# Optimization experiments

Measured on AMD Instinct MI355X. Metric: run time of the kernel, lower is better.

The kernel has to match this reference:

```python
import jax, jax.numpy as jnp
import numpy as np
from jax import lax

NUM_MASK_PARAMS = 67  # 66 weights (64 feat + 2 coord channels) + 1 bias
NUM_GEN_PARAMS = 134


def _coord_maps(h, w, dtype):
    yy = jnp.broadcast_to(jnp.linspace(-1.0, 1.0, h, dtype=dtype)[:, None], (h, w))
    xx = jnp.broadcast_to(jnp.linspace(-1.0, 1.0, w, dtype=dtype)[None, :], (h, w))
    return xx, yy


def _dynamic_head(x_cat, p):
    # x_cat: [66, H, W]; p: [num_ins, 67] -> [num_ins, H, W]
    w = p[:, :NUM_MASK_PARAMS - 1]
    b = p[:, NUM_MASK_PARAMS - 1]
    return jnp.einsum('ic,chw->ihw', w, x_cat) + b[:, None, None]


def setup_inputs() -> dict:
    key = jax.random.key(0)
    ks = jax.random.split(key, 10)
    C, HM, WM, HH, WH, MB, HID = 256, 272, 480, 136, 240, 64, 64
    rn = lambda k, s, sc=1.0: jax.random.normal(k, s, dtype=jnp.float32) * sc
    return {
        'out0': rn(ks[0], (1, C, HM, WM)),
        'out1': rn(ks[1], (1, C, HH, WH)),
        'hm_w': rn(ks[2], (1, C), 0.05),
        'hm_b': jnp.zeros((1,), jnp.float32),
        'params_w': rn(ks[3], (NUM_GEN_PARAMS, C), 0.05),
        'params_b': rn(ks[4], (NUM_GEN_PARAMS,), 0.05),
        'mb_w': rn(ks[5], (MB, C, 3, 3), 0.05),
        'mb_b': jnp.zeros((MB,), jnp.float32),
        'mlp_w1': rn(ks[6], (HM, HID), 0.05),
        'mlp_b1': jnp.zeros((HID,), jnp.float32),
        'mlp_w2': rn(ks[7], (HID, 2), 0.05),
        'mlp_b2': jnp.zeros((2,), jnp.float32),
        'num_ins': 4,
    }


def reference(out0, out1, hm_w, hm_b, params_w, params_b, mb_w, mb_b,
              mlp_w1, mlp_b1, mlp_w2, mlp_b2, num_ins):
    h_mask, w_mask = out0.shape[2], out0.shape[3]
    h_hm, w_hm = out1.shape[2], out1.shape[3]

    # ctnet head: 1x1 convs on the stride-16 feature
    hm = jnp.einsum('kc,bchw->bkhw', hm_w, out1) + hm_b[None, :, None, None]
    params = jnp.einsum('kc,bchw->bkhw', params_w, out1) + params_b[None, :, None, None]
    hm = jnp.clip(jax.nn.sigmoid(hm), 1e-4, 1.0 - 1e-4)  # [1,1,h_hm,w_hm]
    # [1,134,h,w] -> [h*w, 134]
    params_flat = jnp.transpose(params[0], (1, 2, 0)).reshape(-1, NUM_GEN_PARAMS)

    # 3x3 maxpool NMS (stride 1, pad 1), keep only local peaks
    hmax = lax.reduce_window(hm, -jnp.inf, lax.max, (1, 1, 3, 3), (1, 1, 1, 1),
                             [(0, 0), (0, 0), (1, 1), (1, 1)])
    keep = (hmax == hm).astype(hm.dtype)
    heat_nms = (hm * keep).reshape(-1)

    scores, inds = lax.top_k(heat_nms, num_ins)

    # mask branch: 3x3 conv + relu on the stride-8 feature
    mask_branch = lax.conv_general_dilated(out0, mb_w, (1, 1), 'SAME',
                                           dimension_numbers=('NCHW', 'OIHW', 'NCHW'))
    mask_branch = jax.nn.relu(mask_branch + mb_b[None, :, None, None])  # [1,64,H,W]

    xx, yy = _coord_maps(h_mask, w_mask, mask_branch.dtype)
    x_cat = jnp.concatenate([mask_branch[0], xx[None], yy[None]], axis=0)  # [66,H,W]

    gen_params = params_flat[inds]  # [num_ins, 134]
    masks0 = _dynamic_head(x_cat, gen_params[:, :NUM_MASK_PARAMS])   # [num_ins,H,W]
    regs0 = _dynamic_head(x_cat, gen_params[:, NUM_MASK_PARAMS:])    # [num_ins,H,W]

    # row-wise vertical-range MLP over h_mask
    feat_range = jnp.transpose(masks0, (0, 2, 1))  # [num_ins, w_mask, h_mask]
    h1 = jax.nn.relu(feat_range @ mlp_w1 + mlp_b1)
    feat_range = h1 @ mlp_w2 + mlp_b2  # [num_ins, w_mask, 2]

    return scores, inds, regs0, masks0, feat_range
```

## Files before the change

### kernel.cpp

```cpp
#include <hip/hip_runtime.h>
#include <math.h>
#include <limits.h>

#define C_IN 256
#define HM_H 136
#define HM_W 240
#define HM_N (HM_H * HM_W)
#define MB   64
#define MH   272
#define MW   480
#define MN   (MH * MW)
#define NP   134
#define NI   4
#define HID  64

#define REG_OFF   8
#define MASK_OFF  (8 + NI * MN)
#define FEAT_OFF  (8 + 2 * NI * MN)

#define WS_HM   0
#define WS_CV   HM_N
#define WS_CI   (HM_N + 512)
#define WS_GP   (2 * HM_N)
#define WS_WT_F 65824

typedef float  f32x4  __attribute__((ext_vector_type(4)));
typedef short  bf16x8 __attribute__((ext_vector_type(8)));
typedef unsigned short u16x4 __attribute__((ext_vector_type(4)));

__device__ __forceinline__ unsigned short f2bf(float f) {
  unsigned int u = __float_as_uint(f);
  u += 0x7FFFu + ((u >> 16) & 1u);
  return (unsigned short)(u >> 16);
}
__device__ __forceinline__ float b2f(unsigned short h) {
  return __uint_as_float(((unsigned int)h) << 16);
}

__global__ void k_prep(const float* __restrict__ mb_w, unsigned short* __restrict__ wt,
                       const float* __restrict__ out1, const float* __restrict__ hm_w,
                       const float* __restrict__ hm_b, float* __restrict__ ws_hm) {
  __shared__ float part[4][64];
  if (blockIdx.x < 576) {
    int idx = blockIdx.x * 256 + threadIdx.x;
    int j    = idx & 7;
    int lane = (idx >> 3) & 63;
    int nt   = (idx >> 9) & 3;
    int gt   = idx >> 11;
    int t    = gt % 9;
    int g    = gt / 9;
    int n = nt * 16 + (lane & 15);
    int c = g * 32 + (lane >> 4) * 8 + j;
    wt[idx] = f2bf(mb_w[(n * C_IN + c) * 9 + t]);
  } else {
    int b = blockIdx.x - 576, t = threadIdx.x;
    int cg = t >> 6, pl = t & 63;
    int p = b * 64 + pl;
    float s = 0.f;
    #pragma unroll 16
    for (int c = 0; c < 64; ++c)
      s += hm_w[cg * 64 + c] * out1[(cg * 64 + c) * HM_N + p];
    part[cg][pl] = s;
    __syncthreads();
    if (t < 64) {
      float tot = part[0][t] + part[1][t] + part[2][t] + part[3][t] + hm_b[0];
      float sig = 1.f / (1.f + expf(-tot));
      sig = fminf(fmaxf(sig, 1e-4f), 1.f - 1e-4f);
      ws_hm[b * 64 + t] = sig;
    }
  }
}

__device__ __forceinline__ bool better(float av, int ai, float bv, int bi) {
  return (av > bv) || (av == bv && ai < bi);
}

template<int NTHR>
__device__ void top4_tree(float* sv, int* si, int t) {
  for (int s = NTHR / 2; s >= 1; s >>= 1) {
    if (t < s) {
      float a[4], b[4]; int ai[4], bj[4];
      #pragma unroll
      for (int k = 0; k < 4; ++k) {
        a[k] = sv[t * 4 + k];        ai[k] = si[t * 4 + k];
        b[k] = sv[(t + s) * 4 + k];  bj[k] = si[(t + s) * 4 + k];
      }
      float ov[4]; int oi[4];
      int i = 0, j = 0;
      #pragma unroll
      for (int k = 0; k < 4; ++k) {
        if (better(a[i], ai[i], b[j], bj[j])) { ov[k] = a[i]; oi[k] = ai[i]; ++i; }
        else                                   { ov[k] = b[j]; oi[k] = bj[j]; ++j; }
      }
      #pragma unroll
      for (int k = 0; k < 4; ++k) { sv[t * 4 + k] = ov[k]; si[t * 4 + k] = oi[k]; }
    }
    __syncthreads();
  }
}

__global__ void k_nms_top(const float* __restrict__ ws_hm, float* __restrict__ candv,
                          int* __restrict__ candi) {
  __shared__ float sv[256 * 4];
  __shared__ int   si[256 * 4];
  int b = blockIdx.x, t = threadIdx.x;
  float v = -1.f; int idx = INT_MAX;
  if (t < 255) {
    int p = b * 255 + t;
    int y = p / HM_W, x = p - y * HM_W;
    float c = ws_hm[p], m = c;
    #pragma unroll
    for (int dy = -1; dy <= 1; ++dy)
      #pragma unroll
      for (int dx = -1; dx <= 1; ++dx) {
        int yy = y + dy, xx = x + dx;
        if (yy >= 0 && yy < HM_H && xx >= 0 && xx < HM_W)
          m = fmaxf(m, ws_hm[yy * HM_W + xx]);
      }
    v = (c == m) ? c : 0.f;
    idx = p;
  }
  sv[t * 4] = v; si[t * 4] = idx;
  #pragma unroll
  for (int k = 1; k < 4; ++k) { sv[t * 4 + k] = -1.f; si[t * 4 + k] = INT_MAX; }
  __syncthreads();
  top4_tree<256>(sv, si, t);
  if (t == 0) {
    #pragma unroll
    for (int k = 0; k < 4; ++k) { candv[b * 4 + k] = sv[k]; candi[b * 4 + k] = si[k]; }
  }
}

__global__ void k_gen(const float* __restrict__ candv, const int* __restrict__ candi,
                      const float* __restrict__ out1, const float* __restrict__ params_w,
                      const float* __restrict__ params_b, float* __restrict__ ws_gp,
                      float* __restrict__ d_out) {
  __shared__ float sv[128 * 4];
  __shared__ int   si[128 * 4];
  __shared__ float col[C_IN];
  int t = threadIdx.x, i = blockIdx.x;
  if (t < 128) {
    #pragma unroll
    for (int k = 0; k < 4; ++k) { sv[t * 4 + k] = candv[t * 4 + k]; si[t * 4 + k] = candi[t * 4 + k]; }
  }
  __syncthreads();
  top4_tree<128>(sv, si, t);
  if (i == 0 && t < 4) {
    d_out[t]     = sv[t];
    d_out[4 + t] = (float)si[t];
  }
  int p = si[i];
  col[t] = out1[t * HM_N + p];
  __syncthreads();
  if (t < NP) {
    float s = params_b[t];
    #pragma unroll 8
    for (int c = 0; c < C_IN; ++c) s += params_w[t * C_IN + c] * col[c];
    ws_gp[i * NP + t] = s;
  }
}

#define CSU 32
#define RP  36
#define BUFU (10 * RP * CSU)

__device__ __forceinline__ void stage_store(unsigned short* buf, const f32x4* dq,
                                            bool gv, const int* lw, unsigned sm) {
  #pragma unroll
  for (int e = 0; e < 4; ++e) if ((sm >> e) & 1u) {
    u16x4 v;
    v[0] = f2bf(gv ? dq[0][e] : 0.f);
    v[1] = f2bf(gv ? dq[1][e] : 0.f);
    v[2] = f2bf(gv ? dq[2][e] : 0.f);
    v[3] = f2bf(gv ? dq[3][e] : 0.f);
    *(u16x4*)(buf + lw[e]) = v;
  }
}

__global__ __launch_bounds__(512, 3) void k_conv_mfma(
    const float* __restrict__ out0, const unsigned short* __restrict__ wt,
    const float* __restrict__ mb_b, const float* __restrict__ ws_gp,
    float* __restrict__ d_out) {
  __shared__ unsigned short smem[2 * BUFU];

  int tid  = threadIdx.x;
  int lane = tid & 63;
  int wv   = tid >> 6;
  int n15  = lane & 15;
  int kq   = lane >> 4;
  int gx0 = blockIdx.x * 32, gy0 = blockIdx.y * 8;

  int goff[2]; int lws[2][4]; unsigned smask[2]; bool gvld[2];
  #pragma unroll
  for (int kk = 0; kk < 2; ++kk) {
    int u = tid + 512 * kk;
    bool uv = (u < 800);
    int uu = uv ? u : 0;
    int cq  = uu / 100;
    int rem = uu - cq * 100;
    int row = rem / 10;
    int qx  = rem - row * 10;
    int iy  = gy0 + row - 1;
    int ixq = gx0 + 4 * qx - 4;
    bool v = uv && (iy >= 0) && (iy < MH) && (ixq >= 0) && (ixq + 3 < MW);
    gvld[kk] = v;
    goff[kk] = v ? (cq * 4 * MN + iy * MW + ixq) : 0;
    unsigned sm = 0;
    #pragma unroll
    for (int e = 0; e < 4; ++e) {
      int sx = 4 * qx - 3 + e;
      bool s = uv && (sx >= 0) && (sx < RP);
      int sxc = s ? sx : 0;
      int pix = row * RP + sxc;
      int w2  = (pix ^ (pix >> 2)) & 3;
      lws[kk][e] = s ? ((pix << 5) + ((cq ^ (w2 << 1)) << 2)) : 0;
      if (s) sm |= (1u << e);
    }
    smask[kk] = sm;
  }

  int lrd[9];
  #pragma unroll
  for (int t = 0; t < 9; ++t) {
    int ty = t / 3, tx = t - ty * 3;
    int pix = (wv + ty) * RP + n15 + tx;
    int w2  = (pix ^ (pix >> 2)) & 3;
    lrd[t] = (pix << 5) + ((kq ^ w2) << 3);
  }

  {
    f32x4 dq[4];
    {
      const float* sp = out0 + goff[0];
      #pragma unroll
      for (int j = 0; j < 4; ++j) dq[j] = *(const f32x4*)(sp + j * MN);
      stage_store(smem, dq, gvld[0], lws[0], smask[0]);
    }
    if (tid < 288) {
      const float* sp = out0 + goff[1];
      #pragma unroll
      for (int j = 0; j < 4; ++j) dq[j] = *(const f32x4*)(sp + j * MN);
      stage_store(smem, dq, gvld[1], lws[1], smask[1]);
    }
  }
  __syncthreads();

  f32x4 acc[2][4];
  #pragma unroll
  for (int i = 0; i < 2; ++i)
    #pragma unroll
    for (int nt = 0; nt < 4; ++nt)
      acc[i][nt] = (f32x4){0.f, 0.f, 0.f, 0.f};

  #pragma unroll 1
  for (int g = 0; g < 8; ++g) {
    const unsigned short* cur = smem + (g & 1) * BUFU;
    unsigned short*       nxt = smem + ((g + 1) & 1) * BUFU;
    const float*          src = out0 + (g + 1) * (32 * MN);
    f32x4 dqa[4], dqb[4];

    if (g < 7) {
      const float* sp = src + goff[0];
      #pragma unroll
      for (int j = 0; j < 4; ++j) dqa[j] = *(const f32x4*)(sp + j * MN);
    }
    #pragma unroll
    for (int t = 0; t < 4; ++t) {
      const unsigned short* wb = wt + (g * 9 + t) * 2048 + lane * 8;
      bf16x8 bf[4];
      #pragma unroll
      for (int nt = 0; nt < 4; ++nt) bf[nt] = *(const bf16x8*)(wb + nt * 512);
      bf16x8 a0 = *(const bf16x8*)&cur[lrd[t]];
      bf16x8 a1 = *(const bf16x8*)&cur[lrd[t] + 512];
      #pragma unroll
      for (int nt = 0; nt < 4; ++nt) {
        acc[0][nt] = __builtin_amdgcn_mfma_f32_16x16x32_bf16(a0, bf[nt], acc[0][nt], 0, 0, 0);
        acc[1][nt] = __builtin_amdgcn_mfma_f32_16x16x32_bf16(a1, bf[nt], acc[1][nt], 0, 0, 0);
      }
    }
    if (g < 7) {
      stage_store(nxt, dqa, gvld[0], lws[0], smask[0]);
      if (tid < 288) {
        const float* sp = src + goff[1];
        #pragma unroll
        for (int j = 0; j < 4; ++j) dqb[j] = *(const f32x4*)(sp + j * MN);
      }
    }
    #pragma unroll
    for (int t = 4; t < 9; ++t) {
      const unsigned short* wb = wt + (g * 9 + t) * 2048 + lane * 8;
      bf16x8 bf[4];
      #pragma unroll
      for (int nt = 0; nt < 4; ++nt) bf[nt] = *(const bf16x8*)(wb + nt * 512);
      bf16x8 a0 = *(const bf16x8*)&cur[lrd[t]];
      bf16x8 a1 = *(const bf16x8*)&cur[lrd[t] + 512];
      #pragma unroll
      for (int nt = 0; nt < 4; ++nt) {
        acc[0][nt] = __builtin_amdgcn_mfma_f32_16x16x32_bf16(a0, bf[nt], acc[0][nt], 0, 0, 0);
        acc[1][nt] = __builtin_amdgcn_mfma_f32_16x16x32_bf16(a1, bf[nt], acc[1][nt], 0, 0, 0);
      }
    }
    if (g < 7 && tid < 288) stage_store(nxt, dqb, gvld[1], lws[1], smask[1]);
    __syncthreads();
  }

  #define ES 66
  {
    float bias[4];
    #pragma unroll
    for (int nt = 0; nt < 4; ++nt) bias[nt] = mb_b[nt * 16 + n15];
    #pragma unroll
    for (int i = 0; i < 2; ++i) {
      int pbase = wv * 32 + i * 16;
      #pragma unroll
      for (int nt = 0; nt < 4; ++nt)
        #pragma unroll
        for (int reg = 0; reg < 4; ++reg) {
          float vv = fmaxf(acc[i][nt][reg] + bias[nt], 0.f);
          smem[(pbase + kq * 4 + reg) * ES + nt * 16 + n15] = f2bf(vv);
        }
    }
  }
  __syncthreads();

  int p = tid & 255, hh = tid >> 8;
  int ob = hh * 32;
  float mres[4] = {0.f, 0.f, 0.f, 0.f};
  float rres[4] = {0.f, 0.f, 0.f, 0.f};
  #pragma unroll 8
  for (int o = 0; o < 32; ++o) {
    float v = b2f(smem[p * ES + ob + o]);
    #pragma unroll
    for (int i = 0; i < 4; ++i) {
      mres[i] += ws_gp[i * NP + ob + o] * v;
      rres[i] += ws_gp[i * NP + 67 + ob + o] * v;
    }
  }
  float* pf = (float*)smem + 8704;
  if (hh) {
    #pragma unroll
    for (int i = 0; i < 4; ++i) { pf[p * 8 + i] = mres[i]; pf[p * 8 + 4 + i] = rres[i]; }
  }
  __syncthreads();
  if (!hh) {
    int r = p >> 5, xcol = p & 31;
    int gy = gy0 + r, gx = gx0 + xcol;
    float xc = -1.f + (2.f / 479.f) * (float)gx;
    float yc = -1.f + (2.f / 271.f) * (float)gy;
    int pix = gy * MW + gx;
    #pragma unroll
    for (int i = 0; i < 4; ++i) {
      const float* gp = ws_gp + i * NP;
      d_out[MASK_OFF + i * MN + pix] = mres[i] + pf[p * 8 + i]     + gp[66]  + gp[64]  * xc + gp[65]  * yc;
      d_out[REG_OFF  + i * MN + pix] = rres[i] + pf[p * 8 + 4 + i] + gp[133] + gp[131] * xc + gp[132] * yc;
    }
  }
}

__global__ void k_mlp(const float* __restrict__ masks0, const float* __restrict__ w1,
                      const float* __restrict__ b1, const float* __restrict__ w2,
                      const float* __restrict__ b2, float* __restrict__ d_out) {
  int blk = blockIdx.x;
  int i = blk / MW;
  int w = blk - i * MW;
  int k = threadIdx.x;
  const float* mcol = masks0 + i * MN + w;
  float s = b1[k];
  #pragma unroll 4
  for (int h = 0; h < MH; ++h) s += mcol[h * MW] * w1[h * HID + k];
  s = fmaxf(s, 0.f);
  float o0 = s * w2[k * 2 + 0];
  float o1 = s * w2[k * 2 + 1];
  #pragma unroll
  for (int off = 32; off >= 1; off >>= 1) {
    o0 += __shfl_down(o0, off);
    o1 += __shfl_down(o1, off);
  }
  if (k == 0) {
    d_out[FEAT_OFF + blk * 2 + 0] = o0 + b2[0];
    d_out[FEAT_OFF + blk * 2 + 1] = o1 + b2[1];
  }
}

extern "C" void kernel_launch(void* const* d_in, const int* in_sizes, int n_in,
                              void* d_out, int out_size, void* d_ws, size_t ws_size,
                              hipStream_t stream) {
  const float* out0     = (const float*)d_in[0];
  const float* out1     = (const float*)d_in[1];
  const float* hm_w     = (const float*)d_in[2];
  const float* hm_b     = (const float*)d_in[3];
  const float* params_w = (const float*)d_in[4];
  const float* params_b = (const float*)d_in[5];
  const float* mb_w     = (const float*)d_in[6];
  const float* mb_b     = (const float*)d_in[7];
  const float* mlp_w1   = (const float*)d_in[8];
  const float* mlp_b1   = (const float*)d_in[9];
  const float* mlp_w2   = (const float*)d_in[10];
  const float* mlp_b2   = (const float*)d_in[11];

  float* ws      = (float*)d_ws;
  float* ws_hm   = ws + WS_HM;
  float* candv   = ws + WS_CV;
  int*   candi   = (int*)(ws + WS_CI);
  float* ws_gp   = ws + WS_GP;
  unsigned short* ws_wt = (unsigned short*)(ws + WS_WT_F);
  float* out     = (float*)d_out;

  k_prep<<<1086, 256, 0, stream>>>(mb_w, ws_wt, out1, hm_w, hm_b, ws_hm);
  k_nms_top<<<128, 256, 0, stream>>>(ws_hm, candv, candi);
  k_gen<<<NI, 256, 0, stream>>>(candv, candi, out1, params_w, params_b, ws_gp, out);
  dim3 gconv(MW / 32, MH / 8);
  k_conv_mfma<<<gconv, 512, 0, stream>>>(out0, ws_wt, mb_b, ws_gp, out);
  k_mlp<<<NI * MW, 64, 0, stream>>>(out + MASK_OFF, mlp_w1, mlp_b1, mlp_w2, mlp_b2, out);
}
```

Measured before the change: 343.5 us.

## Retile conv MFMA waves across channels and batch 8 columns per MLP block

```diff
diff --git a/kernel.cpp b/kernel.cpp
--- a/kernel.cpp
+++ b/kernel.cpp
@@ -26,7 +26,7 @@
 
 typedef float  f32x4  __attribute__((ext_vector_type(4)));
 typedef short  bf16x8 __attribute__((ext_vector_type(8)));
-typedef unsigned short u16x4 __attribute__((ext_vector_type(4)));
+typedef unsigned short u16x8 __attribute__((ext_vector_type(8)));
 
 __device__ __forceinline__ unsigned short f2bf(float f) {
   unsigned int u = __float_as_uint(f);
@@ -160,24 +160,41 @@
   }
 }
 
-#define CSU 32
-#define RP  36
-#define BUFU (10 * RP * CSU)
-
-__device__ __forceinline__ void stage_store(unsigned short* buf, const f32x4* dq,
-                                            bool gv, const int* lw, unsigned sm) {
+#define RP   36
+#define BUFU (10 * RP * 32)
+
+__device__ __forceinline__ void stage_store8(unsigned short* buf, const f32x4* dq,
+                                             bool gv, const int* lw, unsigned sm) {
   #pragma unroll
   for (int e = 0; e < 4; ++e) if ((sm >> e) & 1u) {
-    u16x4 v;
-    v[0] = f2bf(gv ? dq[0][e] : 0.f);
-    v[1] = f2bf(gv ? dq[1][e] : 0.f);
-    v[2] = f2bf(gv ? dq[2][e] : 0.f);
-    v[3] = f2bf(gv ? dq[3][e] : 0.f);
-    *(u16x4*)(buf + lw[e]) = v;
-  }
-}
-
-__global__ __launch_bounds__(512, 3) void k_conv_mfma(
+    u16x8 v;
+    #pragma unroll
+    for (int j = 0; j < 8; ++j) v[j] = f2bf(gv ? dq[j][e] : 0.f);
+    *(u16x8*)(buf + lw[e]) = v;
+  }
+}
+
+#define MFMA_TAPS(B, T0)                                                         \
+  _Pragma("unroll")                                                              \
+  for (int tt = 0; tt < 3; ++tt) {                                               \
+    unsigned pk = lrdp[(T0) + tt];                                               \
+    const unsigned short* c0 = cur + (pk & 0xFFFFu);                             \
+    const unsigned short* c1 = cur + (pk >> 16);                                 \
+    bf16x8 a0 = *(const bf16x8*)c0;                                              \
+    bf16x8 a1 = *(const bf16x8*)(c0 + 512);                                      \
+    bf16x8 a2 = *(const bf16x8*)c1;                                              \
+    bf16x8 a3 = *(const bf16x8*)(c1 + 512);                                      \
+    acc[0][0] = __builtin_amdgcn_mfma_f32_16x16x32_bf16(a0, B[tt][0], acc[0][0], 0, 0, 0); \
+    acc[0][1] = __builtin_amdgcn_mfma_f32_16x16x32_bf16(a0, B[tt][1], acc[0][1], 0, 0, 0); \
+    acc[1][0] = __builtin_amdgcn_mfma_f32_16x16x32_bf16(a1, B[tt][0], acc[1][0], 0, 0, 0); \
+    acc[1][1] = __builtin_amdgcn_mfma_f32_16x16x32_bf16(a1, B[tt][1], acc[1][1], 0, 0, 0); \
+    acc[2][0] = __builtin_amdgcn_mfma_f32_16x16x32_bf16(a2, B[tt][0], acc[2][0], 0, 0, 0); \
+    acc[2][1] = __builtin_amdgcn_mfma_f32_16x16x32_bf16(a2, B[tt][1], acc[2][1], 0, 0, 0); \
+    acc[3][0] = __builtin_amdgcn_mfma_f32_16x16x32_bf16(a3, B[tt][0], acc[3][0], 0, 0, 0); \
+    acc[3][1] = __builtin_amdgcn_mfma_f32_16x16x32_bf16(a3, B[tt][1], acc[3][1], 0, 0, 0); \
+  }
+
+__global__ __launch_bounds__(512, 4) void k_conv_mfma(
     const float* __restrict__ out0, const unsigned short* __restrict__ wt,
     const float* __restrict__ mb_b, const float* __restrict__ ws_gp,
     float* __restrict__ d_out) {
@@ -188,68 +205,63 @@
   int wv   = tid >> 6;
   int n15  = lane & 15;
   int kq   = lane >> 4;
+  int pg   = wv & 3;
+  int ce   = wv >> 2;
   int gx0 = blockIdx.x * 32, gy0 = blockIdx.y * 8;
 
-  int goff[2]; int lws[2][4]; unsigned smask[2]; bool gvld[2];
-  #pragma unroll
-  for (int kk = 0; kk < 2; ++kk) {
-    int u = tid + 512 * kk;
-    bool uv = (u < 800);
-    int uu = uv ? u : 0;
-    int cq  = uu / 100;
-    int rem = uu - cq * 100;
-    int row = rem / 10;
-    int qx  = rem - row * 10;
-    int iy  = gy0 + row - 1;
-    int ixq = gx0 + 4 * qx - 4;
-    bool v = uv && (iy >= 0) && (iy < MH) && (ixq >= 0) && (ixq + 3 < MW);
-    gvld[kk] = v;
-    goff[kk] = v ? (cq * 4 * MN + iy * MW + ixq) : 0;
-    unsigned sm = 0;
-    #pragma unroll
-    for (int e = 0; e < 4; ++e) {
-      int sx = 4 * qx - 3 + e;
-      bool s = uv && (sx >= 0) && (sx < RP);
-      int sxc = s ? sx : 0;
-      int pix = row * RP + sxc;
-      int w2  = (pix ^ (pix >> 2)) & 3;
-      lws[kk][e] = s ? ((pix << 5) + ((cq ^ (w2 << 1)) << 2)) : 0;
-      if (s) sm |= (1u << e);
-    }
-    smask[kk] = sm;
-  }
-
-  int lrd[9];
+  bool act = tid < 400;
+  int u    = act ? tid : 0;
+  int co8  = u / 100;
+  int rem  = u - co8 * 100;
+  int row  = rem / 10;
+  int qx   = rem - row * 10;
+  int iy   = gy0 + row - 1;
+  int ixq  = gx0 + 4 * qx - 4;
+  bool gvld = act && (iy >= 0) && (iy < MH) && (ixq >= 0) && (ixq + 3 < MW);
+  int goff  = gvld ? (co8 * 8 * MN + iy * MW + ixq) : 0;
+  int lws[4]; unsigned smask = 0;
+  #pragma unroll
+  for (int e = 0; e < 4; ++e) {
+    int sx = 4 * qx - 3 + e;
+    bool sv = act && (sx >= 0) && (sx < RP);
+    int pixw = row * RP + (sv ? sx : 0);
+    int w2 = (pixw ^ (pixw >> 2)) & 3;
+    int q  = (pixw ^ row) & 1;
+    lws[e] = (pixw >> 1) * 64 + ((co8 ^ w2) << 4) + q * 8;
+    if (sv) smask |= (1u << e);
+  }
+
+  unsigned lrdp[9];
   #pragma unroll
   for (int t = 0; t < 9; ++t) {
     int ty = t / 3, tx = t - ty * 3;
-    int pix = (wv + ty) * RP + n15 + tx;
-    int w2  = (pix ^ (pix >> 2)) & 3;
-    lrd[t] = (pix << 5) + ((kq ^ w2) << 3);
+    int sr0 = pg * 2 + ty;
+    int pix0 = sr0 * RP + n15 + tx;
+    int w20 = (pix0 ^ (pix0 >> 2)) & 3;
+    int q0  = (pix0 ^ sr0) & 1;
+    unsigned o0 = (pix0 >> 1) * 64 + ((kq ^ w20) << 4) + q0 * 8;
+    int sr1 = sr0 + 1;
+    int pix1 = sr1 * RP + n15 + tx;
+    int w21 = (pix1 ^ (pix1 >> 2)) & 3;
+    int q1  = (pix1 ^ sr1) & 1;
+    unsigned o1 = (pix1 >> 1) * 64 + ((kq ^ w21) << 4) + q1 * 8;
+    lrdp[t] = o0 | (o1 << 16);
   }
 
   {
-    f32x4 dq[4];
-    {
-      const float* sp = out0 + goff[0];
-      #pragma unroll
-      for (int j = 0; j < 4; ++j) dq[j] = *(const f32x4*)(sp + j * MN);
-      stage_store(smem, dq, gvld[0], lws[0], smask[0]);
-    }
-    if (tid < 288) {
-      const float* sp = out0 + goff[1];
-      #pragma unroll
-      for (int j = 0; j < 4; ++j) dq[j] = *(const f32x4*)(sp + j * MN);
-      stage_store(smem, dq, gvld[1], lws[1], smask[1]);
-    }
-  }
-  __syncthreads();
-
-  f32x4 acc[2][4];
-  #pragma unroll
-  for (int i = 0; i < 2; ++i)
-    #pragma unroll
-    for (int nt = 0; nt < 4; ++nt)
+    f32x4 dq[8];
+    const float* sp = out0 + goff;
+    #pragma unroll
+    for (int j = 0; j < 8; ++j) dq[j] = *(const f32x4*)(sp + j * MN);
+    stage_store8(smem, dq, gvld, lws, smask);
+  }
+  __syncthreads();
+
+  f32x4 acc[4][2];
+  #pragma unroll
+  for (int i = 0; i < 4; ++i)
+    #pragma unroll
+    for (int nt = 0; nt < 2; ++nt)
       acc[i][nt] = (f32x4){0.f, 0.f, 0.f, 0.f};
 
   #pragma unroll 1
@@ -257,67 +269,59 @@
     const unsigned short* cur = smem + (g & 1) * BUFU;
     unsigned short*       nxt = smem + ((g + 1) & 1) * BUFU;
     const float*          src = out0 + (g + 1) * (32 * MN);
-    f32x4 dqa[4], dqb[4];
-
+    const unsigned short* wg_ = wt + g * (9 * 2048) + ce * 1024 + lane * 8;
+
+    bf16x8 b0[3][2], b1[3][2];
+    #pragma unroll
+    for (int tt = 0; tt < 3; ++tt) {
+      b0[tt][0] = *(const bf16x8*)(wg_ + tt * 2048);
+      b0[tt][1] = *(const bf16x8*)(wg_ + tt * 2048 + 512);
+    }
+    #pragma unroll
+    for (int tt = 0; tt < 3; ++tt) {
+      b1[tt][0] = *(const bf16x8*)(wg_ + (3 + tt) * 2048);
+      b1[tt][1] = *(const bf16x8*)(wg_ + (3 + tt) * 2048 + 512);
+    }
+    __builtin_amdgcn_sched_barrier(0);
+    f32x4 dq[8];
     if (g < 7) {
-      const float* sp = src + goff[0];
-      #pragma unroll
-      for (int j = 0; j < 4; ++j) dqa[j] = *(const f32x4*)(sp + j * MN);
-    }
-    #pragma unroll
-    for (int t = 0; t < 4; ++t) {
-      const unsigned short* wb = wt + (g * 9 + t) * 2048 + lane * 8;
-      bf16x8 bf[4];
-      #pragma unroll
-      for (int nt = 0; nt < 4; ++nt) bf[nt] = *(const bf16x8*)(wb + nt * 512);
-      bf16x8 a0 = *(const bf16x8*)&cur[lrd[t]];
-      bf16x8 a1 = *(const bf16x8*)&cur[lrd[t] + 512];
-      #pragma unroll
-      for (int nt = 0; nt < 4; ++nt) {
-        acc[0][nt] = __builtin_amdgcn_mfma_f32_16x16x32_bf16(a0, bf[nt], acc[0][nt], 0, 0, 0);
-        acc[1][nt] = __builtin_amdgcn_mfma_f32_16x16x32_bf16(a1, bf[nt], acc[1][nt], 0, 0, 0);
-      }
-    }
-    if (g < 7) {
-      stage_store(nxt, dqa, gvld[0], lws[0], smask[0]);
-      if (tid < 288) {
-        const float* sp = src + goff[1];
-        #pragma unroll
-        for (int j = 0; j < 4; ++j) dqb[j] = *(const f32x4*)(sp + j * MN);
-      }
-    }
-    #pragma unroll
-    for (int t = 4; t < 9; ++t) {
-      const unsigned short* wb = wt + (g * 9 + t) * 2048 + lane * 8;
-      bf16x8 bf[4];
-      #pragma unroll
-      for (int nt = 0; nt < 4; ++nt) bf[nt] = *(const bf16x8*)(wb + nt * 512);
-      bf16x8 a0 = *(const bf16x8*)&cur[lrd[t]];
-      bf16x8 a1 = *(const bf16x8*)&cur[lrd[t] + 512];
-      #pragma unroll
-      for (int nt = 0; nt < 4; ++nt) {
-        acc[0][nt] = __builtin_amdgcn_mfma_f32_16x16x32_bf16(a0, bf[nt], acc[0][nt], 0, 0, 0);
-        acc[1][nt] = __builtin_amdgcn_mfma_f32_16x16x32_bf16(a1, bf[nt], acc[1][nt], 0, 0, 0);
-      }
-    }
-    if (g < 7 && tid < 288) stage_store(nxt, dqb, gvld[1], lws[1], smask[1]);
+      const float* sp = src + goff;
+      #pragma unroll
+      for (int j = 0; j < 8; ++j) dq[j] = *(const f32x4*)(sp + j * MN);
+    }
+    __builtin_amdgcn_sched_barrier(0);
+
+    MFMA_TAPS(b0, 0)
+    MFMA_TAPS(b1, 3)
+
+    bf16x8 b2[3][2];
+    #pragma unroll
+    for (int tt = 0; tt < 3; ++tt) {
+      b2[tt][0] = *(const bf16x8*)(wg_ + (6 + tt) * 2048);
+      b2[tt][1] = *(const bf16x8*)(wg_ + (6 + tt) * 2048 + 512);
+    }
+    if (g < 7) stage_store8(nxt, dq, gvld, lws, smask);
+
+    MFMA_TAPS(b2, 6)
+
     __syncthreads();
   }
 
   #define ES 66
   {
-    float bias[4];
-    #pragma unroll
-    for (int nt = 0; nt < 4; ++nt) bias[nt] = mb_b[nt * 16 + n15];
-    #pragma unroll
-    for (int i = 0; i < 2; ++i) {
-      int pbase = wv * 32 + i * 16;
-      #pragma unroll
-      for (int nt = 0; nt < 4; ++nt)
+    float bias[2];
+    #pragma unroll
+    for (int nt = 0; nt < 2; ++nt) bias[nt] = mb_b[(ce * 2 + nt) * 16 + n15];
+    #pragma unroll
+    for (int i = 0; i < 4; ++i) {
+      int mt = pg * 4 + i;
+      int pbase = (mt >> 1) * 32 + (mt & 1) * 16;
+      #pragma unroll
+      for (int nt = 0; nt < 2; ++nt)
         #pragma unroll
         for (int reg = 0; reg < 4; ++reg) {
           float vv = fmaxf(acc[i][nt][reg] + bias[nt], 0.f);
-          smem[(pbase + kq * 4 + reg) * ES + nt * 16 + n15] = f2bf(vv);
+          smem[(pbase + kq * 4 + reg) * ES + (ce * 2 + nt) * 16 + n15] = f2bf(vv);
         }
     }
   }
@@ -360,25 +364,44 @@
 __global__ void k_mlp(const float* __restrict__ masks0, const float* __restrict__ w1,
                       const float* __restrict__ b1, const float* __restrict__ w2,
                       const float* __restrict__ b2, float* __restrict__ d_out) {
+  __shared__ float mt[MH][8];
   int blk = blockIdx.x;
-  int i = blk / MW;
-  int w = blk - i * MW;
-  int k = threadIdx.x;
-  const float* mcol = masks0 + i * MN + w;
-  float s = b1[k];
+  int i  = blk / 60;
+  int wg = blk - i * 60;
+  int w0 = wg * 8;
+  int k  = threadIdx.x;
+  const float* mbase = masks0 + i * MN + w0;
   #pragma unroll 4
-  for (int h = 0; h < MH; ++h) s += mcol[h * MW] * w1[h * HID + k];
-  s = fmaxf(s, 0.f);
-  float o0 = s * w2[k * 2 + 0];
-  float o1 = s * w2[k * 2 + 1];
-  #pragma unroll
-  for (int off = 32; off >= 1; off >>= 1) {
-    o0 += __shfl_down(o0, off);
-    o1 += __shfl_down(o1, off);
-  }
-  if (k == 0) {
-    d_out[FEAT_OFF + blk * 2 + 0] = o0 + b2[0];
-    d_out[FEAT_OFF + blk * 2 + 1] = o1 + b2[1];
+  for (int it = 0; it < 34; ++it) {
+    int idx = it * 64 + k;
+    int h = idx >> 3, wj = idx & 7;
+    mt[h][wj] = mbase[h * MW + wj];
+  }
+  __syncthreads();
+  float s[8];
+  #pragma unroll
+  for (int wj = 0; wj < 8; ++wj) s[wj] = b1[k];
+  #pragma unroll 4
+  for (int h = 0; h < MH; ++h) {
+    float wk = w1[h * HID + k];
+    #pragma unroll
+    for (int wj = 0; wj < 8; ++wj) s[wj] += mt[h][wj] * wk;
+  }
+  float w20 = w2[k * 2 + 0], w21 = w2[k * 2 + 1];
+  #pragma unroll
+  for (int wj = 0; wj < 8; ++wj) {
+    float h1 = fmaxf(s[wj], 0.f);
+    float o0 = h1 * w20;
+    float o1 = h1 * w21;
+    #pragma unroll
+    for (int off = 32; off >= 1; off >>= 1) {
+      o0 += __shfl_down(o0, off);
+      o1 += __shfl_down(o1, off);
+    }
+    if (k == 0) {
+      d_out[FEAT_OFF + (i * MW + w0 + wj) * 2 + 0] = o0 + b2[0];
+      d_out[FEAT_OFF + (i * MW + w0 + wj) * 2 + 1] = o1 + b2[1];
+    }
   }
 }
 
@@ -411,5 +434,5 @@
   k_gen<<<NI, 256, 0, stream>>>(candv, candi, out1, params_w, params_b, ws_gp, out);
   dim3 gconv(MW / 32, MH / 8);
   k_conv_mfma<<<gconv, 512, 0, stream>>>(out0, ws_wt, mb_b, ws_gp, out);
-  k_mlp<<<NI * MW, 64, 0, stream>>>(out + MASK_OFF, mlp_w1, mlp_b1, mlp_w2, mlp_b2, out);
-}
+  k_mlp<<<NI * 60, 64, 0, stream>>>(out + MASK_OFF, mlp_w1, mlp_b1, mlp_w2, mlp_b2, out);
+}
```

Result: slower. 383.5 us (+11.6%).
